# Performance work log

Hardware: AMD Instinct MI355X
Metric: run time of the kernel (lower is better)

## Reference

```python
import jax, jax.numpy as jnp
import numpy as np

N0, N1, N2 = 120000, 40000, 10000   # sampled node counts per hop
E0, E1 = 600000, 150000             # edges per block (fanout ~15)
DIN, DH, NC = 128, 256, 47


def _glorot(k, fan_in, fan_out):
    s = (2.0 / (fan_in + fan_out)) ** 0.5
    return jax.random.normal(k, (fan_in, fan_out), jnp.float32) * s


def setup_inputs() -> dict:
    key = jax.random.key(0)
    ks = jax.random.split(key, 20)
    x0 = jax.random.normal(ks[0], (N0, DIN), jnp.float32)
    src0 = jax.random.randint(ks[1], (E0,), 0, N0)
    dst0 = jax.random.randint(ks[2], (E0,), 0, N1)
    src1 = jax.random.randint(ks[3], (E1,), 0, N1)
    dst1 = jax.random.randint(ks[4], (E1,), 0, N2)
    srcb0 = jax.random.randint(ks[5], (E0,), 0, N0)
    dstb0 = jax.random.randint(ks[6], (E0,), 0, N1)
    srcb1 = jax.random.randint(ks[7], (E1,), 0, N1)
    dstb1 = jax.random.randint(ks[8], (E1,), 0, N2)
    # id_old_value_new: must satisfy idx[:n] < n for every truncation length n,
    # i.e. idx[k] in [0, k+1)
    rng = np.random.default_rng(0)
    idx = jnp.asarray((rng.random(N0) * (np.arange(N0) + 1)).astype(np.int64))
    mix_ratio = jnp.float32(0.5)
    Wl0 = _glorot(ks[9], DIN, DH); Wr0 = _glorot(ks[10], DIN, DH)
    b0 = jnp.zeros((DH,), jnp.float32)
    Wl1 = _glorot(ks[11], DH, DH); Wr1 = _glorot(ks[12], DH, DH)
    b1 = jnp.zeros((DH,), jnp.float32)
    Wlin = _glorot(ks[13], DH, NC)
    blin = jnp.zeros((NC,), jnp.float32)
    return dict(x0=x0, src0=src0, dst0=dst0, src1=src1, dst1=dst1,
                srcb0=srcb0, dstb0=dstb0, srcb1=srcb1, dstb1=dstb1,
                idx=idx, mix_ratio=mix_ratio,
                Wl0=Wl0, Wr0=Wr0, b0=b0, Wl1=Wl1, Wr1=Wr1, b1=b1,
                Wlin=Wlin, blin=blin)


def _sage(x_all, root_x, src, dst, n_root, Wl, Wr, b):
    # PyG-style SAGEConv, mean aggregation: lin_l(mean_j x_j) + lin_r(root)
    msgs = x_all[src]                                        # [E, D] gather
    s = jax.ops.segment_sum(msgs, dst, num_segments=n_root)  # [n_root, D]
    cnt = jax.ops.segment_sum(jnp.ones_like(dst, dtype=x_all.dtype), dst,
                              num_segments=n_root)
    mean = s / jnp.maximum(cnt, 1.0)[:, None]
    return mean @ Wl + root_x @ Wr + b


def reference(x0, src0, dst0, src1, dst1, srcb0, dstb0, srcb1, dstb1,
              idx, mix_ratio, Wl0, Wr0, b0, Wl1, Wr1, b1, Wlin, blin):
    blocks = [(src0, dst0, N1), (src1, dst1, N2)]
    blocks_b = [(srcb0, dstb0, N1), (srcb1, dstb1, N2)]
    params = [(Wl0, Wr0, b0), (Wl1, Wr1, b1)]
    m = mix_ratio

    # first branch (dropout omitted: inference mode)
    aggr_xs = [x0]
    for i in range(2):
        src, dst, n_root = blocks[i]
        Wl, Wr, b = params[i]
        root_x = aggr_xs[-1][:n_root]
        x = jax.nn.relu(_sage(aggr_xs[-1], root_x, src, dst, n_root, Wl, Wr, b))
        aggr_xs.append(x)

    # permuted branch via id_old_value_new gather
    aggr_xs_b = [x[idx[: x.shape[0]]] for x in aggr_xs]

    x_mix = aggr_xs[0] * m + aggr_xs_b[0] * (1.0 - m)
    for i in range(2):
        src, dst, n_root = blocks[i]
        srcb, dstb, n_root_b = blocks_b[i]
        Wl, Wr, b = params[i]
        x_new = jax.nn.relu(_sage(aggr_xs[i], x_mix[:n_root], src, dst,
                                  n_root, Wl, Wr, b))
        x_new_b = jax.nn.relu(_sage(aggr_xs_b[i], x_mix[:n_root_b], srcb, dstb,
                                    n_root_b, Wl, Wr, b))
        x_mix = x_new * m + x_new_b * (1.0 - m)

    logits = x_mix @ Wlin + blin
    return jax.nn.log_softmax(logits, axis=-1)
```

## Files before the change

### kernel.cpp

```cpp
#include <hip/hip_runtime.h>
#include <math.h>

#define N1C 40000
#define N2C 10000
#define DIN 128
#define DH  256
#define NC  47

#define TOTCNT (2 * N1C + 2 * N2C)
#define CAP 64
#define CURSTR 16

typedef __attribute__((ext_vector_type(8))) short v8s;
typedef __attribute__((ext_vector_type(4))) float v4f;
typedef __attribute__((ext_vector_type(2))) float v2f;

#if __has_builtin(__builtin_amdgcn_cvt_pk_f32_fp8)
#define HW_FP8 1
#endif

__device__ __forceinline__ unsigned short f2bf(float f) {
    unsigned int u = __float_as_uint(f);
    u += 0x7FFF + ((u >> 16) & 1);
    return (unsigned short)(u >> 16);
}

__device__ __forceinline__ unsigned char f2e4m3(float f) {
    unsigned int u = __float_as_uint(f);
    unsigned char s = (unsigned char)((u >> 24) & 0x80);
    float a = __uint_as_float(u & 0x7FFFFFFF);
    if (a > 448.0f) a = 448.0f;
    if (a < 0.015625f) {
        int k = (int)rintf(a * 512.0f);
        return s | (unsigned char)k;
    }
    unsigned int bits = __float_as_uint(a);
    int et = (int)(bits >> 23) - 127 + 7;
    unsigned int m32 = bits & 0x7FFFFF;
    unsigned int m3 = m32 >> 20;
    unsigned int rest = m32 & 0xFFFFF;
    if (rest > 0x80000 || (rest == 0x80000 && (m3 & 1))) m3++;
    if (m3 == 8) { m3 = 0; et++; }
    if (et > 15 || (et == 15 && m3 == 7)) return s | 0x7E;
    return s | (unsigned char)((et << 3) | m3);
}

__device__ __forceinline__ unsigned int pack4_e4m3(float f0, float f1,
                                                   float f2, float f3) {
#if __has_builtin(__builtin_amdgcn_cvt_pk_fp8_f32)
    int q = __builtin_amdgcn_cvt_pk_fp8_f32(f0, f1, 0, false);
    q = __builtin_amdgcn_cvt_pk_fp8_f32(f2, f3, q, true);
    return (unsigned int)q;
#else
    return (unsigned int)f2e4m3(f0) | ((unsigned int)f2e4m3(f1) << 8) |
           ((unsigned int)f2e4m3(f2) << 16) | ((unsigned int)f2e4m3(f3) << 24);
#endif
}

__device__ __forceinline__ void dec4(unsigned int u, float& f0, float& f1,
                                     float& f2, float& f3) {
#ifdef HW_FP8
    v2f lo = __builtin_amdgcn_cvt_pk_f32_fp8((int)u, false);
    v2f hi = __builtin_amdgcn_cvt_pk_f32_fp8((int)u, true);
    f0 = lo[0]; f1 = lo[1]; f2 = hi[0]; f3 = hi[1];
#else
    auto d1 = [](unsigned int b) -> float {
        int e = (b >> 3) & 15, mm = b & 7;
        float d = (e == 0) ? (float)mm * (1.0f / 512.0f)
                           : (1.0f + (float)mm * 0.125f) * exp2f((float)(e - 7));
        return (b & 0x80) ? -d : d;
    };
    f0 = d1(u & 0xFF); f1 = d1((u >> 8) & 0xFF);
    f2 = d1((u >> 16) & 0xFF); f3 = d1(u >> 24);
#endif
}

__global__ __launch_bounds__(256) void front_fused(
        const int* __restrict__ src0, const int* __restrict__ dst0,
        const int* __restrict__ srcb0, const int* __restrict__ dstb0,
        const int* __restrict__ src1, const int* __restrict__ dst1,
        const int* __restrict__ srcb1, const int* __restrict__ dstb1,
        const int* __restrict__ perm, int* __restrict__ cur,
        int* __restrict__ bucket, int E0, int E1, int nbFill,
        const float* __restrict__ x0, unsigned char* __restrict__ x0f,
        long n8, int nbConv,
        const float* __restrict__ Wl0, const float* __restrict__ Wr0,
        const float* __restrict__ Wl1, const float* __restrict__ Wr1,
        unsigned short* __restrict__ Wt0l, unsigned short* __restrict__ Wt0r,
        unsigned short* __restrict__ Wt1l, unsigned short* __restrict__ Wt1r) {
    int b = blockIdx.x, t = threadIdx.x;
    if (b < nbFill) {
        int tot = 2 * E0 + 2 * E1;
        int base = b * 512;
#pragma unroll
        for (int j = 0; j < 2; j++) {
            int e = base + j * 256 + t;
            if (e < tot) {
                int s, bin;
                if (e < E0) {
                    s = src0[e];                  bin = dst0[e];
                } else if (e < 2 * E0) {
                    int le = e - E0;
                    s = perm[srcb0[le]];          bin = N1C + dstb0[le];
                } else if (e < 2 * E0 + E1) {
                    int le = e - 2 * E0;
                    s = src1[le];                 bin = 2 * N1C + dst1[le];
                } else {
                    int le = e - 2 * E0 - E1;
                    s = perm[srcb1[le]];          bin = 2 * N1C + N2C + dstb1[le];
                }
                int pos = atomicAdd(&cur[(size_t)bin * CURSTR], 1);
                if (pos < CAP) bucket[(size_t)bin * CAP + pos] = s;
            }
        }
    } else if (b < nbFill + nbConv) {
        long i = (long)(b - nbFill) * 256 + t;
        if (i >= n8) return;
        const float4* p = (const float4*)(x0 + i * 8);
        float4 a = p[0], c = p[1];
        uint2 q;
        q.x = pack4_e4m3(a.x, a.y, a.z, a.w);
        q.y = pack4_e4m3(c.x, c.y, c.z, c.w);
        *(uint2*)(x0f + i * 8) = q;
    } else {
        int id = (b - nbFill - nbConv) * 256 + t;
        const int S0 = DIN * DH;
        const int S1 = DH * DH;
        const float* W; unsigned short* Wt; int K, loc;
        if (id < S0)                   { W = Wl0; Wt = Wt0l; K = DIN; loc = id; }
        else if (id < 2 * S0)          { W = Wr0; Wt = Wt0r; K = DIN; loc = id - S0; }
        else if (id < 2 * S0 + S1)     { W = Wl1; Wt = Wt1l; K = DH;  loc = id - 2 * S0; }
        else if (id < 2 * S0 + 2 * S1) { W = Wr1; Wt = Wt1r; K = DH;  loc = id - 2 * S0 - S1; }
        else return;
        int n = loc / K, k = loc - n * K;
        Wt[(size_t)n * K + k] = f2bf(W[(size_t)k * DH + n]);
    }
}

__global__ __launch_bounds__(256) void gather_mean_128f(
        const unsigned char* __restrict__ xf, const int* __restrict__ bucket,
        const int* __restrict__ cur, unsigned short* __restrict__ mean0,
        unsigned short* __restrict__ meanb0) {
    const int half = N1C / 8;
    int b = blockIdx.x;
    int binbase; unsigned short* outp; int rb;
    if (b < half) { binbase = 0;   outp = mean0;  rb = b; }
    else          { binbase = N1C; outp = meanb0; rb = b - half; }
    int wv = threadIdx.x >> 6, lane = threadIdx.x & 63;
    int row = rb * 8 + wv * 2 + (lane >> 5);
    int c4 = (lane & 31) * 4;
    int bin = binbase + row;
    int cnt = min(cur[(size_t)bin * CURSTR], CAP);
    const int* cs = bucket + (size_t)bin * CAP;
    float a0 = 0.0f, a1 = 0.0f, a2 = 0.0f, a3 = 0.0f;
    int i = 0;
    for (; i + 3 < cnt; i += 4) {
        int s0 = cs[i], s1 = cs[i + 1], s2 = cs[i + 2], s3 = cs[i + 3];
        unsigned int u = *(const unsigned int*)&xf[(size_t)s0 * DIN + c4];
        unsigned int v = *(const unsigned int*)&xf[(size_t)s1 * DIN + c4];
        unsigned int w = *(const unsigned int*)&xf[(size_t)s2 * DIN + c4];
        unsigned int z = *(const unsigned int*)&xf[(size_t)s3 * DIN + c4];
        float u0, u1, u2, u3, w0, w1, w2, w3, p0, p1, p2, p3, q0, q1, q2, q3;
        dec4(u, u0, u1, u2, u3);
        dec4(v, w0, w1, w2, w3);
        dec4(w, p0, p1, p2, p3);
        dec4(z, q0, q1, q2, q3);
        a0 += (u0 + w0) + (p0 + q0); a1 += (u1 + w1) + (p1 + q1);
        a2 += (u2 + w2) + (p2 + q2); a3 += (u3 + w3) + (p3 + q3);
    }
    for (; i < cnt; i++) {
        unsigned int u = *(const unsigned int*)&xf[(size_t)cs[i] * DIN + c4];
        float u0, u1, u2, u3;
        dec4(u, u0, u1, u2, u3);
        a0 += u0; a1 += u1; a2 += u2; a3 += u3;
    }
    float inv = 1.0f / (float)max(cnt, 1);
    uint2 o;
    o.x = (unsigned int)f2bf(a0 * inv) | ((unsigned int)f2bf(a1 * inv) << 16);
    o.y = (unsigned int)f2bf(a2 * inv) | ((unsigned int)f2bf(a3 * inv) << 16);
    *(uint2*)&outp[(size_t)row * DIN + c4] = o;
}

__global__ __launch_bounds__(256) void gather_mean_256f(
        const unsigned char* __restrict__ xf, const int* __restrict__ bucket,
        const int* __restrict__ cur, unsigned short* __restrict__ mean1,
        unsigned short* __restrict__ meanb1) {
    const int half = N2C / 4;
    int b = blockIdx.x;
    int binbase; unsigned short* outp; int rb;
    if (b < half) { binbase = 2 * N1C;       outp = mean1;  rb = b; }
    else          { binbase = 2 * N1C + N2C; outp = meanb1; rb = b - half; }
    int row = rb * 4 + (threadIdx.x >> 6);
    int lane = threadIdx.x & 63;
    int bin = binbase + row;
    int cnt = min(cur[(size_t)bin * CURSTR], CAP);
    const int* cs = bucket + (size_t)bin * CAP;
    float a0 = 0.0f, a1 = 0.0f, a2 = 0.0f, a3 = 0.0f;
    int i = 0;
    for (; i + 3 < cnt; i += 4) {
        int s0 = cs[i], s1 = cs[i + 1], s2 = cs[i + 2], s3 = cs[i + 3];
        unsigned int u = *(const unsigned int*)&xf[(size_t)s0 * DH + lane * 4];
        unsigned int v = *(const unsigned int*)&xf[(size_t)s1 * DH + lane * 4];
        unsigned int w = *(const unsigned int*)&xf[(size_t)s2 * DH + lane * 4];
        unsigned int z = *(const unsigned int*)&xf[(size_t)s3 * DH + lane * 4];
        float u0, u1, u2, u3, w0, w1, w2, w3, p0, p1, p2, p3, q0, q1, q2, q3;
        dec4(u, u0, u1, u2, u3);
        dec4(v, w0, w1, w2, w3);
        dec4(w, p0, p1, p2, p3);
        dec4(z, q0, q1, q2, q3);
        a0 += (u0 + w0) + (p0 + q0); a1 += (u1 + w1) + (p1 + q1);
        a2 += (u2 + w2) + (p2 + q2); a3 += (u3 + w3) + (p3 + q3);
    }
    for (; i < cnt; i++) {
        unsigned int u = *(const unsigned int*)&xf[(size_t)cs[i] * DH + lane * 4];
        float u0, u1, u2, u3;
        dec4(u, u0, u1, u2, u3);
        a0 += u0; a1 += u1; a2 += u2; a3 += u3;
    }
    float inv = 1.0f / (float)max(cnt, 1);
    uint2 o;
    o.x = (unsigned int)f2bf(a0 * inv) | ((unsigned int)f2bf(a1 * inv) << 16);
    o.y = (unsigned int)f2bf(a2 * inv) | ((unsigned int)f2bf(a3 * inv) << 16);
    *(uint2*)&outp[(size_t)row * DH + lane * 4] = o;
}

#define KP0 136
#define H0T 5
__global__ __launch_bounds__(256, 2) void hop0_mfma(
        const float* __restrict__ x0, const int* __restrict__ idx,
        const unsigned short* __restrict__ mean0, const unsigned short* __restrict__ meanb0,
        const unsigned short* __restrict__ Wtl, const unsigned short* __restrict__ Wtr,
        const float* __restrict__ b, const float* __restrict__ mixp,
        unsigned char* __restrict__ x1f, unsigned short* __restrict__ xm1) {
    __shared__ unsigned short Alds[4][16][KP0];
    int t = threadIdx.x;
    int wv = t >> 6, lane = t & 63;
    int mrow = lane & 15, quad = lane >> 4;
    float m = *mixp;

    v8s wl[4][4], wr[4][4];
    float bb[4];
#pragma unroll
    for (int ct = 0; ct < 4; ct++) {
        int n = wv * 64 + mrow * 4 + ct;
        bb[ct] = b[n];
#pragma unroll
        for (int ks = 0; ks < 4; ks++) {
            int k0 = ks * 32 + quad * 8;
            wl[ct][ks] = *(const v8s*)&Wtl[(size_t)n * DIN + k0];
            wr[ct][ks] = *(const v8s*)&Wtr[(size_t)n * DIN + k0];
        }
    }

    for (int tile = 0; tile < H0T; tile++) {
        int row0 = (blockIdx.x * H0T + tile) * 16;
        {
            int r = t >> 4, k0 = (t & 15) * 8;
            int rg = row0 + r;
            *(v8s*)&Alds[0][r][k0] = *(const v8s*)&mean0[(size_t)rg * DIN + k0];
            *(v8s*)&Alds[1][r][k0] = *(const v8s*)&meanb0[(size_t)rg * DIN + k0];
            const float4* xr4 = (const float4*)&x0[(size_t)rg * DIN + k0];
            float4 A0 = xr4[0], A1 = xr4[1];
            int ib = idx[rg];
            const float4* xb4 = (const float4*)&x0[(size_t)ib * DIN + k0];
            float4 B0 = xb4[0], B1 = xb4[1];
            float fa[8] = {A0.x, A0.y, A0.z, A0.w, A1.x, A1.y, A1.z, A1.w};
            float fb[8] = {B0.x, B0.y, B0.z, B0.w, B1.x, B1.y, B1.z, B1.w};
            v8s vr, vm;
#pragma unroll
            for (int j = 0; j < 8; j++) {
                vr[j] = (short)f2bf(fa[j]);
                vm[j] = (short)f2bf(m * fa[j] + (1.0f - m) * fb[j]);
            }
            *(v8s*)&Alds[2][r][k0] = vr;
            *(v8s*)&Alds[3][r][k0] = vm;
        }
        __syncthreads();
        v4f accA[4], accB[4], accC[4], accD[4];
#pragma unroll
        for (int ct = 0; ct < 4; ct++) {
            accA[ct] = (v4f){0.f, 0.f, 0.f, 0.f}; accB[ct] = (v4f){0.f, 0.f, 0.f, 0.f};
            accC[ct] = (v4f){0.f, 0.f, 0.f, 0.f}; accD[ct] = (v4f){0.f, 0.f, 0.f, 0.f};
        }
#pragma unroll
        for (int ks = 0; ks < 4; ks++) {
            int k0 = ks * 32 + quad * 8;
            v8s aM = *(v8s*)&Alds[0][mrow][k0];
            v8s aB = *(v8s*)&Alds[1][mrow][k0];
            v8s aR = *(v8s*)&Alds[2][mrow][k0];
            v8s aX = *(v8s*)&Alds[3][mrow][k0];
#pragma unroll
            for (int ct = 0; ct < 4; ct++) {
                accA[ct] = __builtin_amdgcn_mfma_f32_16x16x32_bf16(aM, wl[ct][ks], accA[ct], 0, 0, 0);
                accB[ct] = __builtin_amdgcn_mfma_f32_16x16x32_bf16(aB, wl[ct][ks], accB[ct], 0, 0, 0);
                accC[ct] = __builtin_amdgcn_mfma_f32_16x16x32_bf16(aR, wr[ct][ks], accC[ct], 0, 0, 0);
                accD[ct] = __builtin_amdgcn_mfma_f32_16x16x32_bf16(aX, wr[ct][ks], accD[ct], 0, 0, 0);
            }
        }
        int colb = wv * 64 + mrow * 4;
#pragma unroll
        for (int r = 0; r < 4; r++) {
            int row = row0 + quad * 4 + r;
            float xv[4];
            unsigned short sh[4];
#pragma unroll
            for (int ct = 0; ct < 4; ct++) {
                float pA = accA[ct][r], pB = accB[ct][r], pC = accC[ct][r], pD = accD[ct][r];
                xv[ct]    = fmaxf(pA + pC + bb[ct], 0.0f);
                float xn  = fmaxf(pA + pD + bb[ct], 0.0f);
                float xnb = fmaxf(pB + pD + bb[ct], 0.0f);
                sh[ct] = f2bf(m * xn + (1.0f - m) * xnb);
            }
            unsigned int xpack = pack4_e4m3(xv[0], xv[1], xv[2], xv[3]);
            unsigned int s01 = (unsigned int)sh[0] | ((unsigned int)sh[1] << 16);
            unsigned int s23 = (unsigned int)sh[2] | ((unsigned int)sh[3] << 16);
            *(unsigned int*)&x1f[(size_t)row * DH + colb] = xpack;
            uint2 xm = {s01, s23};
            *(uint2*)&xm1[(size_t)row * DH + colb] = xm;
        }
        __syncthreads();
    }
}

#define KP1 264
#define H1T 2
__global__ __launch_bounds__(256, 2) void hop1_mfma(
        const unsigned short* __restrict__ mean1, const unsigned short* __restrict__ meanb1,
        const unsigned short* __restrict__ xm1,
        const unsigned short* __restrict__ Wtl, const unsigned short* __restrict__ Wtr,
        const float* __restrict__ b, const float* __restrict__ mixp,
        float* __restrict__ xm2) {
    __shared__ unsigned short Alds[3][16][KP1];
    int t = threadIdx.x;
    int wv = t >> 6, lane = t & 63;
    int mrow = lane & 15, quad = lane >> 4;
    float m = *mixp;

    v8s wlc[4][4], wrc[4][4];
    float bb[4];
#pragma unroll
    for (int ct = 0; ct < 4; ct++) {
        int n = wv * 64 + mrow * 4 + ct;
        bb[ct] = b[n];
#pragma unroll
        for (int ks = 0; ks < 4; ks++) {
            int k0 = ks * 32 + quad * 8;
            wlc[ct][ks] = *(const v8s*)&Wtl[(size_t)n * DH + k0];
            wrc[ct][ks] = *(const v8s*)&Wtr[(size_t)n * DH + k0];
        }
    }

    for (int tt = 0; tt < H1T; tt++) {
        int tIdx = blockIdx.x * H1T + tt;
        if (tIdx >= N2C / 16) break;
        int row0 = tIdx * 16;
        {
            int r = t >> 4, k0 = (t & 15) * 16;
            int rg = row0 + r;
            *(v8s*)&Alds[0][r][k0]     = *(const v8s*)&mean1[(size_t)rg * DH + k0];
            *(v8s*)&Alds[0][r][k0 + 8] = *(const v8s*)&mean1[(size_t)rg * DH + k0 + 8];
            *(v8s*)&Alds[1][r][k0]     = *(const v8s*)&meanb1[(size_t)rg * DH + k0];
            *(v8s*)&Alds[1][r][k0 + 8] = *(const v8s*)&meanb1[(size_t)rg * DH + k0 + 8];
            *(v8s*)&Alds[2][r][k0]     = *(const v8s*)&xm1[(size_t)rg * DH + k0];
            *(v8s*)&Alds[2][r][k0 + 8] = *(const v8s*)&xm1[(size_t)rg * DH + k0 + 8];
        }
        __syncthreads();
        v4f accA[4], accB[4], accC[4];
#pragma unroll
        for (int ct = 0; ct < 4; ct++) {
            accA[ct] = (v4f){0.f, 0.f, 0.f, 0.f};
            accB[ct] = (v4f){0.f, 0.f, 0.f, 0.f};
            accC[ct] = (v4f){0.f, 0.f, 0.f, 0.f};
        }
#pragma unroll
        for (int ks = 0; ks < 8; ks++) {
            int k0 = ks * 32 + quad * 8;
            v8s aM = *(v8s*)&Alds[0][mrow][k0];
            v8s aB = *(v8s*)&Alds[1][mrow][k0];
            v8s aR = *(v8s*)&Alds[2][mrow][k0];
#pragma unroll
            for (int ct = 0; ct < 4; ct++) {
                v8s bl, br;
                if (ks < 4) { bl = wlc[ct][ks]; br = wrc[ct][ks]; }
                else {
                    int n = wv * 64 + mrow * 4 + ct;
                    bl = *(const v8s*)&Wtl[(size_t)n * DH + k0];
                    br = *(const v8s*)&Wtr[(size_t)n * DH + k0];
                }
                accA[ct] = __builtin_amdgcn_mfma_f32_16x16x32_bf16(aM, bl, accA[ct], 0, 0, 0);
                accB[ct] = __builtin_amdgcn_mfma_f32_16x16x32_bf16(aB, bl, accB[ct], 0, 0, 0);
                accC[ct] = __builtin_amdgcn_mfma_f32_16x16x32_bf16(aR, br, accC[ct], 0, 0, 0);
            }
        }
        int colb = wv * 64 + mrow * 4;
#pragma unroll
        for (int r = 0; r < 4; r++) {
            int row = row0 + quad * 4 + r;
            float4 o;
            float v0 = fmaxf(accA[0][r] + accC[0][r] + bb[0], 0.0f);
            float w0 = fmaxf(accB[0][r] + accC[0][r] + bb[0], 0.0f);
            float v1 = fmaxf(accA[1][r] + accC[1][r] + bb[1], 0.0f);
            float w1 = fmaxf(accB[1][r] + accC[1][r] + bb[1], 0.0f);
            float v2 = fmaxf(accA[2][r] + accC[2][r] + bb[2], 0.0f);
            float w2 = fmaxf(accB[2][r] + accC[2][r] + bb[2], 0.0f);
            float v3 = fmaxf(accA[3][r] + accC[3][r] + bb[3], 0.0f);
            float w3 = fmaxf(accB[3][r] + accC[3][r] + bb[3], 0.0f);
            o.x = m * v0 + (1.0f - m) * w0;
            o.y = m * v1 + (1.0f - m) * w1;
            o.z = m * v2 + (1.0f - m) * w2;
            o.w = m * v3 + (1.0f - m) * w3;
            *(float4*)&xm2[(size_t)row * DH + colb] = o;
        }
        __syncthreads();
    }
}

__global__ __launch_bounds__(256) void logits_lsm(
        const float* __restrict__ xmix2, const float* __restrict__ Wlin,
        const float* __restrict__ blin, float* __restrict__ out, int nrows) {
    int w = threadIdx.x >> 6;
    int row = blockIdx.x * 4 + w;
    int t = threadIdx.x & 63;
    __shared__ float xs[4][DH];
    if (row < nrows)
        for (int i = t; i < DH; i += 64) xs[w][i] = xmix2[(size_t)row * DH + i];
    __syncthreads();
    if (row >= nrows) return;
    float acc = 0.0f;
    if (t < NC) {
        acc = blin[t];
        for (int k = 0; k < DH; k++) acc += xs[w][k] * Wlin[k * NC + t];
    }
    float v = (t < NC) ? acc : -INFINITY;
    float mx = v;
    for (int off = 32; off; off >>= 1) mx = fmaxf(mx, __shfl_xor(mx, off, 64));
    float ex = (t < NC) ? expf(acc - mx) : 0.0f;
    float sum = ex;
    for (int off = 32; off; off >>= 1) sum += __shfl_xor(sum, off, 64);
    if (t < NC) out[(size_t)row * NC + t] = acc - mx - logf(sum);
}

extern "C" void kernel_launch(void* const* d_in, const int* in_sizes, int n_in,
                              void* d_out, int out_size, void* d_ws, size_t ws_size,
                              hipStream_t stream) {
    const float* x0    = (const float*)d_in[0];
    const int*   src0  = (const int*)d_in[1];
    const int*   dst0  = (const int*)d_in[2];
    const int*   src1  = (const int*)d_in[3];
    const int*   dst1  = (const int*)d_in[4];
    const int*   srcb0 = (const int*)d_in[5];
    const int*   dstb0 = (const int*)d_in[6];
    const int*   srcb1 = (const int*)d_in[7];
    const int*   dstb1 = (const int*)d_in[8];
    const int*   idx   = (const int*)d_in[9];
    const float* mixp  = (const float*)d_in[10];
    const float* Wl0   = (const float*)d_in[11];
    const float* Wr0   = (const float*)d_in[12];
    const float* b0    = (const float*)d_in[13];
    const float* Wl1   = (const float*)d_in[14];
    const float* Wr1   = (const float*)d_in[15];
    const float* b1    = (const float*)d_in[16];
    const float* Wlin  = (const float*)d_in[17];
    const float* blin  = (const float*)d_in[18];
    float* out = (float*)d_out;

    const int E0 = in_sizes[1];
    const int E1 = in_sizes[3];
    const long x0elems = (long)in_sizes[0];

    int* wsi    = (int*)d_ws;
    int* cur    = wsi;
    int* bucket = cur + (size_t)TOTCNT * CURSTR;
    unsigned short* wsh = (unsigned short*)(bucket + (size_t)TOTCNT * CAP);
    unsigned short* mean0  = wsh;
    unsigned short* meanb0 = mean0  + (size_t)N1C * DIN;
    unsigned short* mean1  = meanb0 + (size_t)N1C * DIN;
    unsigned short* meanb1 = mean1  + (size_t)N2C * DH;
    unsigned short* xm1h   = meanb1 + (size_t)N2C * DH;
    unsigned short* Wt0l   = xm1h   + (size_t)N1C * DH;
    unsigned short* Wt0r   = Wt0l + DIN * DH;
    unsigned short* Wt1l   = Wt0r + DIN * DH;
    unsigned short* Wt1r   = Wt1l + DH * DH;
    float* xm2 = (float*)(Wt1r + DH * DH);
    unsigned char* x0f = (unsigned char*)(xm2 + (size_t)N2C * DH);
    unsigned char* x1f = x0f + (size_t)x0elems;

    hipMemsetAsync(cur, 0, sizeof(int) * (size_t)TOTCNT * CURSTR, stream);

    int etot = 2 * E0 + 2 * E1;
    int nbFill = (etot + 511) / 512;
    long n8 = x0elems / 8;
    int nbConv = (int)((n8 + 255) / 256);
    int nbW = (2 * DIN * DH + 2 * DH * DH + 255) / 256;
    front_fused<<<nbFill + nbConv + nbW, 256, 0, stream>>>(
        src0, dst0, srcb0, dstb0, src1, dst1, srcb1, dstb1, idx, cur, bucket,
        E0, E1, nbFill, x0, x0f, n8, nbConv,
        Wl0, Wr0, Wl1, Wr1, Wt0l, Wt0r, Wt1l, Wt1r);

    gather_mean_128f<<<2 * (N1C / 8), 256, 0, stream>>>(x0f, bucket, cur, mean0, meanb0);

    hop0_mfma<<<N1C / (16 * H0T), 256, 0, stream>>>(x0, idx, mean0, meanb0, Wt0l, Wt0r,
                                                    b0, mixp, x1f, xm1h);

    gather_mean_256f<<<2 * (N2C / 4), 256, 0, stream>>>(x1f, bucket, cur, mean1, meanb1);

    hop1_mfma<<<(N2C / 16 + H1T - 1) / H1T, 256, 0, stream>>>(mean1, meanb1, xm1h,
                                                              Wt1l, Wt1r, b1, mixp, xm2);

    logits_lsm<<<(N2C + 3) / 4, 256, 0, stream>>>(xm2, Wlin, blin, out, N2C);
}
```

Baseline: 336.0 us.

## Fuse neighbor mean gathers into hop MFMA kernels via LDS

Removes the standalone gather_mean kernels and computes the per-row neighbor means for both branches directly inside the hop0 and hop1 MFMA kernels. The bf16 results go straight into the LDS A-tiles. This drops two launches and the global write and reread of the mean buffers. In exchange the gather latency now sits inside the matmul kernels, which run fewer blocks (500 and 313) under launch bounds of 2, so the latency-bound gathers may get less parallelism and could stall the MFMA work.

```diff
diff --git a/kernel.cpp b/kernel.cpp
--- a/kernel.cpp
+++ b/kernel.cpp
@@ -73,6 +73,34 @@
     f0 = d1(u & 0xFF); f1 = d1((u >> 8) & 0xFF);
     f2 = d1((u >> 16) & 0xFF); f3 = d1(u >> 24);
 #endif
+}
+
+__device__ __forceinline__ void gather_acc(const unsigned char* __restrict__ xf,
+                                           const int* __restrict__ cs, int cnt,
+                                           int D, int c4,
+                                           float& a0, float& a1, float& a2, float& a3) {
+    a0 = a1 = a2 = a3 = 0.0f;
+    int i = 0;
+    for (; i + 3 < cnt; i += 4) {
+        int s0 = cs[i], s1 = cs[i + 1], s2 = cs[i + 2], s3 = cs[i + 3];
+        unsigned int u = *(const unsigned int*)&xf[(size_t)s0 * D + c4];
+        unsigned int v = *(const unsigned int*)&xf[(size_t)s1 * D + c4];
+        unsigned int w = *(const unsigned int*)&xf[(size_t)s2 * D + c4];
+        unsigned int z = *(const unsigned int*)&xf[(size_t)s3 * D + c4];
+        float u0, u1, u2, u3, w0, w1, w2, w3, p0, p1, p2, p3, q0, q1, q2, q3;
+        dec4(u, u0, u1, u2, u3);
+        dec4(v, w0, w1, w2, w3);
+        dec4(w, p0, p1, p2, p3);
+        dec4(z, q0, q1, q2, q3);
+        a0 += (u0 + w0) + (p0 + q0); a1 += (u1 + w1) + (p1 + q1);
+        a2 += (u2 + w2) + (p2 + q2); a3 += (u3 + w3) + (p3 + q3);
+    }
+    for (; i < cnt; i++) {
+        unsigned int u = *(const unsigned int*)&xf[(size_t)cs[i] * D + c4];
+        float u0, u1, u2, u3;
+        dec4(u, u0, u1, u2, u3);
+        a0 += u0; a1 += u1; a2 += u2; a3 += u3;
+    }
 }
 
 __global__ __launch_bounds__(256) void front_fused(
@@ -137,98 +165,12 @@
     }
 }
 
-__global__ __launch_bounds__(256) void gather_mean_128f(
-        const unsigned char* __restrict__ xf, const int* __restrict__ bucket,
-        const int* __restrict__ cur, unsigned short* __restrict__ mean0,
-        unsigned short* __restrict__ meanb0) {
-    const int half = N1C / 8;
-    int b = blockIdx.x;
-    int binbase; unsigned short* outp; int rb;
-    if (b < half) { binbase = 0;   outp = mean0;  rb = b; }
-    else          { binbase = N1C; outp = meanb0; rb = b - half; }
-    int wv = threadIdx.x >> 6, lane = threadIdx.x & 63;
-    int row = rb * 8 + wv * 2 + (lane >> 5);
-    int c4 = (lane & 31) * 4;
-    int bin = binbase + row;
-    int cnt = min(cur[(size_t)bin * CURSTR], CAP);
-    const int* cs = bucket + (size_t)bin * CAP;
-    float a0 = 0.0f, a1 = 0.0f, a2 = 0.0f, a3 = 0.0f;
-    int i = 0;
-    for (; i + 3 < cnt; i += 4) {
-        int s0 = cs[i], s1 = cs[i + 1], s2 = cs[i + 2], s3 = cs[i + 3];
-        unsigned int u = *(const unsigned int*)&xf[(size_t)s0 * DIN + c4];
-        unsigned int v = *(const unsigned int*)&xf[(size_t)s1 * DIN + c4];
-        unsigned int w = *(const unsigned int*)&xf[(size_t)s2 * DIN + c4];
-        unsigned int z = *(const unsigned int*)&xf[(size_t)s3 * DIN + c4];
-        float u0, u1, u2, u3, w0, w1, w2, w3, p0, p1, p2, p3, q0, q1, q2, q3;
-        dec4(u, u0, u1, u2, u3);
-        dec4(v, w0, w1, w2, w3);
-        dec4(w, p0, p1, p2, p3);
-        dec4(z, q0, q1, q2, q3);
-        a0 += (u0 + w0) + (p0 + q0); a1 += (u1 + w1) + (p1 + q1);
-        a2 += (u2 + w2) + (p2 + q2); a3 += (u3 + w3) + (p3 + q3);
-    }
-    for (; i < cnt; i++) {
-        unsigned int u = *(const unsigned int*)&xf[(size_t)cs[i] * DIN + c4];
-        float u0, u1, u2, u3;
-        dec4(u, u0, u1, u2, u3);
-        a0 += u0; a1 += u1; a2 += u2; a3 += u3;
-    }
-    float inv = 1.0f / (float)max(cnt, 1);
-    uint2 o;
-    o.x = (unsigned int)f2bf(a0 * inv) | ((unsigned int)f2bf(a1 * inv) << 16);
-    o.y = (unsigned int)f2bf(a2 * inv) | ((unsigned int)f2bf(a3 * inv) << 16);
-    *(uint2*)&outp[(size_t)row * DIN + c4] = o;
-}
-
-__global__ __launch_bounds__(256) void gather_mean_256f(
-        const unsigned char* __restrict__ xf, const int* __restrict__ bucket,
-        const int* __restrict__ cur, unsigned short* __restrict__ mean1,
-        unsigned short* __restrict__ meanb1) {
-    const int half = N2C / 4;
-    int b = blockIdx.x;
-    int binbase; unsigned short* outp; int rb;
-    if (b < half) { binbase = 2 * N1C;       outp = mean1;  rb = b; }
-    else          { binbase = 2 * N1C + N2C; outp = meanb1; rb = b - half; }
-    int row = rb * 4 + (threadIdx.x >> 6);
-    int lane = threadIdx.x & 63;
-    int bin = binbase + row;
-    int cnt = min(cur[(size_t)bin * CURSTR], CAP);
-    const int* cs = bucket + (size_t)bin * CAP;
-    float a0 = 0.0f, a1 = 0.0f, a2 = 0.0f, a3 = 0.0f;
-    int i = 0;
-    for (; i + 3 < cnt; i += 4) {
-        int s0 = cs[i], s1 = cs[i + 1], s2 = cs[i + 2], s3 = cs[i + 3];
-        unsigned int u = *(const unsigned int*)&xf[(size_t)s0 * DH + lane * 4];
-        unsigned int v = *(const unsigned int*)&xf[(size_t)s1 * DH + lane * 4];
-        unsigned int w = *(const unsigned int*)&xf[(size_t)s2 * DH + lane * 4];
-        unsigned int z = *(const unsigned int*)&xf[(size_t)s3 * DH + lane * 4];
-        float u0, u1, u2, u3, w0, w1, w2, w3, p0, p1, p2, p3, q0, q1, q2, q3;
-        dec4(u, u0, u1, u2, u3);
-        dec4(v, w0, w1, w2, w3);
-        dec4(w, p0, p1, p2, p3);
-        dec4(z, q0, q1, q2, q3);
-        a0 += (u0 + w0) + (p0 + q0); a1 += (u1 + w1) + (p1 + q1);
-        a2 += (u2 + w2) + (p2 + q2); a3 += (u3 + w3) + (p3 + q3);
-    }
-    for (; i < cnt; i++) {
-        unsigned int u = *(const unsigned int*)&xf[(size_t)cs[i] * DH + lane * 4];
-        float u0, u1, u2, u3;
-        dec4(u, u0, u1, u2, u3);
-        a0 += u0; a1 += u1; a2 += u2; a3 += u3;
-    }
-    float inv = 1.0f / (float)max(cnt, 1);
-    uint2 o;
-    o.x = (unsigned int)f2bf(a0 * inv) | ((unsigned int)f2bf(a1 * inv) << 16);
-    o.y = (unsigned int)f2bf(a2 * inv) | ((unsigned int)f2bf(a3 * inv) << 16);
-    *(uint2*)&outp[(size_t)row * DH + lane * 4] = o;
-}
-
 #define KP0 136
 #define H0T 5
-__global__ __launch_bounds__(256, 2) void hop0_mfma(
+__global__ __launch_bounds__(256, 2) void hop0_fused(
         const float* __restrict__ x0, const int* __restrict__ idx,
-        const unsigned short* __restrict__ mean0, const unsigned short* __restrict__ meanb0,
+        const unsigned char* __restrict__ x0f, const int* __restrict__ bucket,
+        const int* __restrict__ cur,
         const unsigned short* __restrict__ Wtl, const unsigned short* __restrict__ Wtr,
         const float* __restrict__ b, const float* __restrict__ mixp,
         unsigned char* __restrict__ x1f, unsigned short* __restrict__ xm1) {
@@ -236,6 +178,8 @@
     int t = threadIdx.x;
     int wv = t >> 6, lane = t & 63;
     int mrow = lane & 15, quad = lane >> 4;
+    int hw = t >> 5, hl = t & 31;
+    int c4 = hl * 4;
     float m = *mixp;
 
     v8s wl[4][4], wr[4][4];
@@ -257,8 +201,6 @@
         {
             int r = t >> 4, k0 = (t & 15) * 8;
             int rg = row0 + r;
-            *(v8s*)&Alds[0][r][k0] = *(const v8s*)&mean0[(size_t)rg * DIN + k0];
-            *(v8s*)&Alds[1][r][k0] = *(const v8s*)&meanb0[(size_t)rg * DIN + k0];
             const float4* xr4 = (const float4*)&x0[(size_t)rg * DIN + k0];
             float4 A0 = xr4[0], A1 = xr4[1];
             int ib = idx[rg];
@@ -274,6 +216,21 @@
             }
             *(v8s*)&Alds[2][r][k0] = vr;
             *(v8s*)&Alds[3][r][k0] = vm;
+        }
+#pragma unroll
+        for (int rr = 0; rr < 4; rr++) {
+            int task = rr * 8 + hw;
+            int r = task & 15, kind = task >> 4;
+            int bin = (kind ? N1C : 0) + row0 + r;
+            int cnt = min(cur[(size_t)bin * CURSTR], CAP);
+            const int* cs = bucket + (size_t)bin * CAP;
+            float a0, a1, a2, a3;
+            gather_acc(x0f, cs, cnt, DIN, c4, a0, a1, a2, a3);
+            float inv = 1.0f / (float)max(cnt, 1);
+            uint2 o;
+            o.x = (unsigned int)f2bf(a0 * inv) | ((unsigned int)f2bf(a1 * inv) << 16);
+            o.y = (unsigned int)f2bf(a2 * inv) | ((unsigned int)f2bf(a3 * inv) << 16);
+            *(uint2*)&Alds[kind][r][c4] = o;
         }
         __syncthreads();
         v4f accA[4], accB[4], accC[4], accD[4];
@@ -324,8 +281,9 @@
 
 #define KP1 264
 #define H1T 2
-__global__ __launch_bounds__(256, 2) void hop1_mfma(
-        const unsigned short* __restrict__ mean1, const unsigned short* __restrict__ meanb1,
+__global__ __launch_bounds__(256, 2) void hop1_fused(
+        const unsigned char* __restrict__ x1f, const int* __restrict__ bucket,
+        const int* __restrict__ cur,
         const unsigned short* __restrict__ xm1,
         const unsigned short* __restrict__ Wtl, const unsigned short* __restrict__ Wtr,
         const float* __restrict__ b, const float* __restrict__ mixp,
@@ -357,12 +315,23 @@
         {
             int r = t >> 4, k0 = (t & 15) * 16;
             int rg = row0 + r;
-            *(v8s*)&Alds[0][r][k0]     = *(const v8s*)&mean1[(size_t)rg * DH + k0];
-            *(v8s*)&Alds[0][r][k0 + 8] = *(const v8s*)&mean1[(size_t)rg * DH + k0 + 8];
-            *(v8s*)&Alds[1][r][k0]     = *(const v8s*)&meanb1[(size_t)rg * DH + k0];
-            *(v8s*)&Alds[1][r][k0 + 8] = *(const v8s*)&meanb1[(size_t)rg * DH + k0 + 8];
             *(v8s*)&Alds[2][r][k0]     = *(const v8s*)&xm1[(size_t)rg * DH + k0];
             *(v8s*)&Alds[2][r][k0 + 8] = *(const v8s*)&xm1[(size_t)rg * DH + k0 + 8];
+        }
+#pragma unroll
+        for (int rr = 0; rr < 8; rr++) {
+            int task = rr * 4 + wv;
+            int r = task & 15, kind = task >> 4;
+            int bin = 2 * N1C + (kind ? N2C : 0) + row0 + r;
+            int cnt = min(cur[(size_t)bin * CURSTR], CAP);
+            const int* cs = bucket + (size_t)bin * CAP;
+            float a0, a1, a2, a3;
+            gather_acc(x1f, cs, cnt, DH, lane * 4, a0, a1, a2, a3);
+            float inv = 1.0f / (float)max(cnt, 1);
+            uint2 o;
+            o.x = (unsigned int)f2bf(a0 * inv) | ((unsigned int)f2bf(a1 * inv) << 16);
+            o.y = (unsigned int)f2bf(a2 * inv) | ((unsigned int)f2bf(a3 * inv) << 16);
+            *(uint2*)&Alds[kind][r][lane * 4] = o;
         }
         __syncthreads();
         v4f accA[4], accB[4], accC[4];
@@ -472,11 +441,7 @@
     int* cur    = wsi;
     int* bucket = cur + (size_t)TOTCNT * CURSTR;
     unsigned short* wsh = (unsigned short*)(bucket + (size_t)TOTCNT * CAP);
-    unsigned short* mean0  = wsh;
-    unsigned short* meanb0 = mean0  + (size_t)N1C * DIN;
-    unsigned short* mean1  = meanb0 + (size_t)N1C * DIN;
-    unsigned short* meanb1 = mean1  + (size_t)N2C * DH;
-    unsigned short* xm1h   = meanb1 + (size_t)N2C * DH;
+    unsigned short* xm1h   = wsh;
     unsigned short* Wt0l   = xm1h   + (size_t)N1C * DH;
     unsigned short* Wt0r   = Wt0l + DIN * DH;
     unsigned short* Wt1l   = Wt0r + DIN * DH;
@@ -497,15 +462,11 @@
         E0, E1, nbFill, x0, x0f, n8, nbConv,
         Wl0, Wr0, Wl1, Wr1, Wt0l, Wt0r, Wt1l, Wt1r);
 
-    gather_mean_128f<<<2 * (N1C / 8), 256, 0, stream>>>(x0f, bucket, cur, mean0, meanb0);
-
-    hop0_mfma<<<N1C / (16 * H0T), 256, 0, stream>>>(x0, idx, mean0, meanb0, Wt0l, Wt0r,
-                                                    b0, mixp, x1f, xm1h);
-
-    gather_mean_256f<<<2 * (N2C / 4), 256, 0, stream>>>(x1f, bucket, cur, mean1, meanb1);
-
-    hop1_mfma<<<(N2C / 16 + H1T - 1) / H1T, 256, 0, stream>>>(mean1, meanb1, xm1h,
-                                                              Wt1l, Wt1r, b1, mixp, xm2);
+    hop0_fused<<<N1C / (16 * H0T), 256, 0, stream>>>(x0, idx, x0f, bucket, cur,
+                                                     Wt0l, Wt0r, b0, mixp, x1f, xm1h);
+
+    hop1_fused<<<(N2C / 16 + H1T - 1) / H1T, 256, 0, stream>>>(x1f, bucket, cur, xm1h,
+                                                               Wt1l, Wt1r, b1, mixp, xm2);
 
     logits_lsm<<<(N2C + 3) / 4, 256, 0, stream>>>(xm2, Wlin, blin, out, N2C);
 }
```

After: 431.2 us. 1.28x slower.
